# Kernel tuning notes

Measured on AMD Instinct MI355X. Metric: run time of the kernel, lower is better.

The kernel has to match this reference:

```python
import jax, jax.numpy as jnp
import numpy as np

N = 50000        # num_nodes
E = 800000       # num edges (avg degree 16)
R = 8            # num_relations
D_IN = 128       # input_dim
D_H = 128        # gnn_dim
D_OUT = 128      # embed_dim
NUM_DRUGS = 4000 # nodes with node_type == 0 used for pairing
P = 8192         # number of drug pairs (edge_filter columns)


def setup_inputs() -> dict:
    key = jax.random.key(0)
    ks = jax.random.split(key, 24)
    s = 0.05

    def w(k, shape):
        return jax.random.normal(k, shape, jnp.float32) * s

    inp = {
        "x": jax.random.normal(ks[0], (N, D_IN), jnp.float32),
        "edge_index": jax.random.randint(ks[1], (2, E), 0, N),
        "edge_type": jax.random.randint(ks[2], (E,), 0, R),
        "node_type": jax.random.randint(ks[3], (N,), 0, 2),
        "edge_filter": jax.random.randint(ks[4], (2, P), 0, NUM_DRUGS),
        # RGCN layer 1/2/3: per-relation weights, root weight, bias
        "W1": w(ks[5], (R, D_IN, D_H)), "root1": w(ks[6], (D_IN, D_H)), "b1": jnp.zeros((D_H,), jnp.float32),
        "W2": w(ks[7], (R, D_H, D_H)),  "root2": w(ks[8], (D_H, D_H)),  "b2": jnp.zeros((D_H,), jnp.float32),
        "W3": w(ks[9], (R, D_H, D_H)),  "root3": w(ks[10], (D_H, D_H)), "b3": jnp.zeros((D_H,), jnp.float32),
        # ComboMLP: Bilinear(d,d,d) + 3-layer MLP
        "bil_W": w(ks[11], (D_H, D_H, D_H)), "bil_b": jnp.zeros((D_H,), jnp.float32),
        "m1_W": w(ks[12], (D_H, D_H)), "m1_b": jnp.zeros((D_H,), jnp.float32),
        "m2_W": w(ks[13], (D_H, D_H)), "m2_b": jnp.zeros((D_H,), jnp.float32),
        "m3_W": w(ks[14], (D_H, D_OUT)), "m3_b": jnp.zeros((D_OUT,), jnp.float32),
    }
    return inp


def _rgcn_layer(x, src, dst, etype, W, root, b):
    # PyG RGCNConv with aggr='mean': per relation r, mean of neighbor
    # features over incoming rel-r edges, transformed by W[r]; plus root + bias.
    d = x.shape[1]
    msgs = x[src]                                   # [E, d] gather
    seg = dst * R + etype                           # per-(node, relation) segment id
    agg = jax.ops.segment_sum(msgs, seg, num_segments=N * R).reshape(N, R, d)
    cnt = jax.ops.segment_sum(jnp.ones_like(etype, jnp.float32), seg,
                              num_segments=N * R).reshape(N, R, 1)
    mean = agg / jnp.maximum(cnt, 1.0)              # nodes w/o rel-r edges -> 0
    return jnp.einsum('nrd,rde->ne', mean, W) + x @ root + b


def reference(x, edge_index, edge_type, node_type, edge_filter,
              W1, root1, b1, W2, root2, b2, W3, root3, b3,
              bil_W, bil_b, m1_W, m1_b, m2_W, m2_b, m3_W, m3_b):
    src, dst = edge_index[0], edge_index[1]
    h = jax.nn.relu(_rgcn_layer(x, src, dst, edge_type, W1, root1, b1))
    h = jax.nn.relu(_rgcn_layer(h, src, dst, edge_type, W2, root2, b2))
    h = jax.nn.relu(_rgcn_layer(h, src, dst, edge_type, W3, root3, b3))

    # drug_embeds = kg_out[where(node_type == 0)] (fixed-size for jit)
    drug_idx = jnp.nonzero(node_type == 0, size=NUM_DRUGS, fill_value=0)[0]
    drug = h[drug_idx]                              # [NUM_DRUGS, d]
    fa = drug[edge_filter[0]]                       # [P, d]
    fb = drug[edge_filter[1]]                       # [P, d]

    # torch.nn.Bilinear: out[p,o] = fa[p] @ bil_W[o] @ fb[p] + bil_b[o]
    x_ab = jax.nn.relu(jnp.einsum('pi,oij,pj->po', fa, bil_W, fb) + bil_b)
    x_ab = jax.nn.relu(x_ab @ m1_W + m1_b)
    x_ab = jax.nn.relu(x_ab @ m2_W + m2_b)
    return x_ab @ m3_W + m3_b                       # [P, D_OUT]
```

## Files before the change

### kernel.cpp

```cpp
#include <hip/hip_runtime.h>
#include <hip/hip_bf16.h>

typedef unsigned short ushort_t;
typedef __attribute__((ext_vector_type(8))) short short8v;
typedef __attribute__((ext_vector_type(4))) float f32x4;
typedef __attribute__((ext_vector_type(4))) int int4v;

#define NN 50000
#define EE 800000
#define RRR 8
#define DD 128
#define NDRUG 4000
#define PPAIR 8192
#define BML 32
#define AFS 1160

__device__ __forceinline__ float bf2f(ushort_t u) {
    unsigned int v = ((unsigned int)u) << 16;
    float f; __builtin_memcpy(&f, &v, 4); return f;
}
__device__ __forceinline__ ushort_t f2bf(float f) {
    unsigned int b; __builtin_memcpy(&b, &f, 4);
    unsigned int r = (b + 0x7FFFu + ((b >> 16) & 1u)) >> 16;
    return (ushort_t)r;
}
__device__ __forceinline__ unsigned int pkbf(float lo, float hi) {
    unsigned int r;
    asm("v_cvt_pk_bf16_f32 %0, %1, %2" : "=v"(r) : "v"(lo), "v"(hi));
    return r;
}


__global__ __launch_bounds__(256) void k_count(const int* __restrict__ ei,
                                               const int* __restrict__ et,
                                               int* __restrict__ cnt) {
    int e = blockIdx.x * 256 + threadIdx.x;
    if (e < EE) {
        int dst = ei[EE + e];
        atomicAdd(&cnt[dst * RRR + et[e]], 1);
    }
}

__global__ __launch_bounds__(256) void k_inv_indeg(const int* __restrict__ cnt,
                                                   float* __restrict__ inv,
                                                   int* __restrict__ indeg) {
    int n = blockIdx.x * 256 + threadIdx.x;
    if (n < NN) {
        int s = 0;
#pragma unroll
        for (int r = 0; r < RRR; r++) {
            int c = cnt[n * RRR + r];
            s += c;
            inv[n * RRR + r] = 1.0f / (float)(c > 0 ? c : 1);
        }
        indeg[n] = s;
    }
}

__global__ __launch_bounds__(1024) void k_scan_sel(const int* __restrict__ indeg,
                                                   const int* __restrict__ ntype,
                                                   int* __restrict__ offs,
                                                   int* __restrict__ cursor,
                                                   int* __restrict__ didx) {
    __shared__ int w1[16], w2[16];
    __shared__ int sb1, sb2;
    int tid = threadIdx.x, wid = tid >> 6, lane = tid & 63;
    if (tid == 0) { sb1 = 0; sb2 = 0; }
    __syncthreads();
    for (int c0 = 0; c0 < NN; c0 += 1024) {
        int i = c0 + tid;
        int a0 = (i < NN) ? indeg[i] : 0;
        int b0 = (i < NN && ntype[i] == 0) ? 1 : 0;
        int a = a0, b = b0;
#pragma unroll
        for (int off = 1; off < 64; off <<= 1) {
            int ua = __shfl_up(a, off);
            int ub = __shfl_up(b, off);
            if (lane >= off) { a += ua; b += ub; }
        }
        if (lane == 63) { w1[wid] = a; w2[wid] = b; }
        __syncthreads();
        if (wid == 0) {
            int wa = (lane < 16) ? w1[lane] : 0;
            int wb = (lane < 16) ? w2[lane] : 0;
#pragma unroll
            for (int off = 1; off < 16; off <<= 1) {
                int ua = __shfl_up(wa, off);
                int ub = __shfl_up(wb, off);
                if (lane >= off) { wa += ua; wb += ub; }
            }
            if (lane < 16) { w1[lane] = wa; w2[lane] = wb; }
        }
        __syncthreads();
        int ea = sb1 + (wid ? w1[wid - 1] : 0) + (a - a0);
        int eb = sb2 + (wid ? w2[wid - 1] : 0) + (b - b0);
        if (i < NN) { offs[i] = ea; cursor[i] = ea; }
        if (b0 && eb < NDRUG) didx[eb] = i;
        __syncthreads();
        if (tid == 0) { sb1 += w1[15]; sb2 += w2[15]; }
        __syncthreads();
    }
    if (tid == 0) offs[NN] = sb1;
}

__global__ __launch_bounds__(256) void k_scatter(const int* __restrict__ ei,
                                                 const int* __restrict__ et,
                                                 int* __restrict__ cursor,
                                                 int* __restrict__ sorted) {
    int e = blockIdx.x * 256 + threadIdx.x;
    if (e < EE) {
        int dst = ei[EE + e];
        int pos = atomicAdd(&cursor[dst], 1);
        sorted[pos] = ei[e] | (et[e] << 20);
    }
}


__global__ __launch_bounds__(256) void k_cvt(const float* __restrict__ src,
                                             ushort_t* __restrict__ dst, int n4) {
    int i = blockIdx.x * 256 + threadIdx.x;
    if (i < n4) {
        float4 v = ((const float4*)src)[i];
        uint2 o;
        o.x = (unsigned int)f2bf(v.x) | ((unsigned int)f2bf(v.y) << 16);
        o.y = (unsigned int)f2bf(v.z) | ((unsigned int)f2bf(v.w) << 16);
        ((uint2*)dst)[i] = o;
    }
}

__global__ __launch_bounds__(256) void k_prep_wcat(const float* __restrict__ W8,
                                                   const float* __restrict__ root,
                                                   ushort_t* __restrict__ dst) {
    int idx = blockIdx.x * 256 + threadIdx.x;
    if (idx < 144 * 128 * 8) {
        int e = idx & 7, col = (idx >> 3) & 127, ko = idx >> 10;
        int k = ko * 8 + e, slab = k >> 7, kk = k & 127;
        const float* src = (slab < 8) ? (W8 + slab * 16384) : root;
        dst[idx] = f2bf(src[kk * 128 + col]);
    }
}

__global__ __launch_bounds__(256) void k_prep_w(const float* __restrict__ root,
                                                ushort_t* __restrict__ dst) {
    int idx = blockIdx.x * 256 + threadIdx.x;
    if (idx < 16384) {
        int col = idx >> 7, kk = idx & 127;
        dst[idx] = f2bf(root[kk * 128 + col]);
    }
}

__global__ __launch_bounds__(256) void k_prep_wb3(const float* __restrict__ bilW,
                                                  ushort_t* __restrict__ dst) {
    int idx = blockIdx.x * 256 + threadIdx.x;
    if (idx < 2097152) {
        int e = idx & 7, o = (idx >> 3) & 127, ko = idx >> 10;
        dst[idx] = f2bf(bilW[(size_t)o * 16384 + ko * 8 + e]);
    }
}

__global__ __launch_bounds__(512) void k_layer(const ushort_t* __restrict__ hin,
                                               const ushort_t* __restrict__ WcatT,
                                               const float* __restrict__ bias,
                                               const float* __restrict__ inv,
                                               const int* __restrict__ offs,
                                               const int* __restrict__ sorted,
                                               ushort_t* __restrict__ hout) {
    __shared__ short Af[BML * AFS];
    int tid = threadIdx.x;
    int n0 = blockIdx.x * BML;
    int node = tid >> 4, tsub = tid & 15;
    int n = n0 + node;

    float acc[8][8];
#pragma unroll
    for (int r = 0; r < 8; r++)
#pragma unroll
        for (int q = 0; q < 8; q++) acc[r][q] = 0.f;
    short8v hv = {0, 0, 0, 0, 0, 0, 0, 0};

    if (n < NN) {
        hv = ((const short8v*)hin)[(size_t)n * 16 + tsub];
        int e0 = offs[n], e1 = offs[n + 1];
        for (int e = e0; e < e1; e++) {
            int pk = sorted[e];
            int src = pk & 0xFFFFF;
            int et = pk >> 20;
            union { int4v v; short s[8]; } u;
            u.v = ((const int4v*)hin)[(size_t)src * 16 + tsub];
            float v[8];
#pragma unroll
            for (int q = 0; q < 8; q++) v[q] = bf2f((ushort_t)u.s[q]);
#define CASE_R(R) case R: _Pragma("unroll") for (int q = 0; q < 8; q++) acc[R][q] += v[q]; break;
            switch (et) {
                CASE_R(0) CASE_R(1) CASE_R(2) CASE_R(3)
                CASE_R(4) CASE_R(5) CASE_R(6) CASE_R(7)
            }
#undef CASE_R
        }
    }
    int nc = (n < NN) ? n : (NN - 1);
#pragma unroll
    for (int slab = 0; slab < 8; slab++) {
        float sc = (n < NN) ? inv[nc * 8 + slab] : 0.f;
        union { unsigned int u[4]; short8v v; } cv;
        cv.u[0] = pkbf(acc[slab][0] * sc, acc[slab][1] * sc);
        cv.u[1] = pkbf(acc[slab][2] * sc, acc[slab][3] * sc);
        cv.u[2] = pkbf(acc[slab][4] * sc, acc[slab][5] * sc);
        cv.u[3] = pkbf(acc[slab][6] * sc, acc[slab][7] * sc);
        *(short8v*)&Af[node * AFS + slab * 128 + tsub * 8] = cv.v;
    }
    *(short8v*)&Af[node * AFS + 1024 + tsub * 8] = hv;
    __syncthreads();

    int wid = tid >> 6, lane = tid & 63, lo = lane & 15, hi = lane >> 4;
    int rhalf = wid & 1, cgrp = wid >> 1;
    int arow = rhalf * 16 + lo;
    f32x4 a0v = {0.f, 0.f, 0.f, 0.f}, a1v = {0.f, 0.f, 0.f, 0.f};
    const int4v* Bg = (const int4v*)WcatT;
#pragma unroll
    for (int kc = 0; kc < 9; kc++) {
#pragma unroll
        for (int s = 0; s < 4; s++) {
            short8v a = *(const short8v*)&Af[arow * AFS + kc * 128 + s * 32 + hi * 8];
            int ko = kc * 16 + s * 4 + hi;
            union { int4v i; short8v s8; } b0, b1;
            b0.i = Bg[ko * 128 + cgrp * 32 + lo];
            b1.i = Bg[ko * 128 + cgrp * 32 + 16 + lo];
            a0v = __builtin_amdgcn_mfma_f32_16x16x32_bf16(a, b0.s8, a0v, 0, 0, 0);
            a1v = __builtin_amdgcn_mfma_f32_16x16x32_bf16(a, b1.s8, a1v, 0, 0, 0);
        }
    }
#pragma unroll
    for (int q = 0; q < 4; q++) {
        int r = n0 + rhalf * 16 + hi * 4 + q;
        if (r < NN) {
            int c = cgrp * 32 + lo;
            float v0 = fmaxf(a0v[q] + bias[c], 0.f);
            float v1 = fmaxf(a1v[q] + bias[c + 16], 0.f);
            hout[(size_t)r * 128 + c] = f2bf(v0);
            hout[(size_t)r * 128 + c + 16] = f2bf(v1);
        }
    }
}

__global__ __launch_bounds__(256) void k_mfma_nn(const ushort_t* __restrict__ A,
                                                 const ushort_t* __restrict__ Wt,
                                                 const float* __restrict__ bias,
                                                 ushort_t* __restrict__ outb,
                                                 float* __restrict__ outf,
                                                 int M, int nMblk, int relu) {
    __shared__ short As[64 * 136];
    __shared__ short Bs[128 * 136];
    int tid = threadIdx.x;
    int mblk = blockIdx.x % nMblk;
    int row0 = mblk * 64;

    const int4v* Ag = (const int4v*)A;
    int4v* AsV = (int4v*)As;
    for (int idx = tid; idx < 1024; idx += 256) {
        int row = idx >> 4, ck = idx & 15;
        int grow = row0 + row;
        int4v v = {0, 0, 0, 0};
        if (grow < M) v = Ag[(size_t)grow * 16 + ck];
        AsV[row * 17 + ck] = v;
    }
    const int4v* Wg = (const int4v*)Wt;
    int4v* BsV = (int4v*)Bs;
    for (int idx = tid; idx < 2048; idx += 256) {
        int col = idx >> 4, ck = idx & 15;
        BsV[col * 17 + ck] = Wg[idx];
    }
    __syncthreads();

    int wid = tid >> 6, lane = tid & 63, lo = lane & 15, hi = lane >> 4;
    int wrow0 = wid * 16;
    f32x4 acc[8];
#pragma unroll
    for (int t = 0; t < 8; t++) acc[t] = (f32x4)(0.f);

#pragma unroll
    for (int s = 0; s < 4; ++s) {
        short8v a = *(const short8v*)&As[(wrow0 + lo) * 136 + s * 32 + hi * 8];
#pragma unroll
        for (int t = 0; t < 8; t++) {
            short8v b = *(const short8v*)&Bs[(t * 16 + lo) * 136 + s * 32 + hi * 8];
            acc[t] = __builtin_amdgcn_mfma_f32_16x16x32_bf16(a, b, acc[t], 0, 0, 0);
        }
    }

#pragma unroll
    for (int t = 0; t < 8; t++) {
        int col = t * 16 + lo;
        float bs = bias ? bias[col] : 0.f;
#pragma unroll
        for (int q = 0; q < 4; q++) {
            int grow = row0 + wrow0 + hi * 4 + q;
            if (grow < M) {
                float v = acc[t][q] + bs;
                if (relu) v = fmaxf(v, 0.f);
                size_t oidx = (size_t)grow * 128 + col;
                if (outb) outb[oidx] = f2bf(v);
                else      outf[oidx] = v;
            }
        }
    }
}

__global__ __launch_bounds__(512) void k_bil(const ushort_t* __restrict__ hb,
                                             const int* __restrict__ didx,
                                             const int* __restrict__ efil,
                                             const ushort_t* __restrict__ Wb,
                                             const float* __restrict__ bilb,
                                             ushort_t* __restrict__ xab) {
    __shared__ __align__(16) char smem[65536];
    __shared__ int pa[32], pb[32];
    float* faT = (float*)smem;
    float* fbF = (float*)(smem + 16896);
    int tid = threadIdx.x;
    int p0 = blockIdx.x * 32;

    if (tid < 32) pa[tid] = didx[efil[p0 + tid]];
    else if (tid < 64) pb[tid - 32] = didx[efil[PPAIR + p0 + tid - 32]];
    __syncthreads();

    {
        int p = tid >> 4, c8 = tid & 15;
        const int4v* hg = (const int4v*)hb;
        union { int4v v; short s[8]; } ra, rb;
        ra.v = hg[(size_t)pa[p] * 16 + c8];
        rb.v = hg[(size_t)pb[p] * 16 + c8];
        float4* fb4 = (float4*)fbF;
        float4 f0, f1;
        f0.x = bf2f((ushort_t)rb.s[0]); f0.y = bf2f((ushort_t)rb.s[1]);
        f0.z = bf2f((ushort_t)rb.s[2]); f0.w = bf2f((ushort_t)rb.s[3]);
        f1.x = bf2f((ushort_t)rb.s[4]); f1.y = bf2f((ushort_t)rb.s[5]);
        f1.z = bf2f((ushort_t)rb.s[6]); f1.w = bf2f((ushort_t)rb.s[7]);
        fb4[p * 33 + c8 * 2] = f0;
        fb4[p * 33 + c8 * 2 + 1] = f1;
#pragma unroll
        for (int j = 0; j < 8; j++)
            faT[(c8 * 8 + j) * 33 + p] = bf2f((ushort_t)ra.s[j]);
    }
    __syncthreads();

    int wid = tid >> 6, lane = tid & 63, lo = lane & 15, hi = lane >> 4;
    const int4v* Wbg = (const int4v*)Wb;
    const float4* fb4 = (const float4*)fbF;

    f32x4 acc0[8], acc1[8];
#pragma unroll
    for (int t = 0; t < 8; t++) { acc0[t] = (f32x4)(0.f); acc1[t] = (f32x4)(0.f); }

    for (int s = 0; s < 64; ++s) {
        int ko = (wid << 8) + (s << 2) + hi;
        int4v braw[8];
#pragma unroll
        for (int t = 0; t < 8; t++)
            braw[t] = Wbg[ko * 128 + t * 16 + lo];

        int i = (wid << 4) + (s >> 2);
        int jc4 = ((s & 3) << 3) + (hi << 1);
        short8v afr0, afr1;
#pragma unroll
        for (int mi = 0; mi < 2; ++mi) {
            int prow = (mi << 4) + lo;
            float fa = faT[i * 33 + prow];
            float4 f0 = fb4[prow * 33 + jc4];
            float4 f1 = fb4[prow * 33 + jc4 + 1];
            union { unsigned int u[4]; short8v v; } cv;
            cv.u[0] = pkbf(fa * f0.x, fa * f0.y);
            cv.u[1] = pkbf(fa * f0.z, fa * f0.w);
            cv.u[2] = pkbf(fa * f1.x, fa * f1.y);
            cv.u[3] = pkbf(fa * f1.z, fa * f1.w);
            if (mi == 0) afr0 = cv.v; else afr1 = cv.v;
        }
#pragma unroll
        for (int t = 0; t < 8; t++) {
            union { int4v i4; short8v s8; } bb; bb.i4 = braw[t];
            acc0[t] = __builtin_amdgcn_mfma_f32_16x16x32_bf16(afr0, bb.s8, acc0[t], 0, 0, 0);
            acc1[t] = __builtin_amdgcn_mfma_f32_16x16x32_bf16(afr1, bb.s8, acc1[t], 0, 0, 0);
        }
    }
    __syncthreads();

    float* redF = (float*)smem;
    if (wid >= 4) {
        float* r = redF + (wid - 4) * 4096;
#pragma unroll
        for (int t = 0; t < 8; t++)
#pragma unroll
            for (int q = 0; q < 4; q++) {
                r[(hi * 4 + q) * 128 + t * 16 + lo] = acc0[t][q];
                r[(16 + hi * 4 + q) * 128 + t * 16 + lo] = acc1[t][q];
            }
    }
    __syncthreads();
    if (wid < 4) {
        float* r = redF + wid * 4096;
#pragma unroll
        for (int t = 0; t < 8; t++)
#pragma unroll
            for (int q = 0; q < 4; q++) {
                acc0[t][q] += r[(hi * 4 + q) * 128 + t * 16 + lo];
                acc1[t][q] += r[(16 + hi * 4 + q) * 128 + t * 16 + lo];
            }
    }
    __syncthreads();
    if (wid < 4) {
        float* r = redF + wid * 4096;
#pragma unroll
        for (int t = 0; t < 8; t++)
#pragma unroll
            for (int q = 0; q < 4; q++) {
                r[(hi * 4 + q) * 128 + t * 16 + lo] = acc0[t][q];
                r[(16 + hi * 4 + q) * 128 + t * 16 + lo] = acc1[t][q];
            }
    }
    __syncthreads();
    for (int idx = tid; idx < 4096; idx += 512) {
        float s = redF[idx] + redF[4096 + idx] + redF[8192 + idx] + redF[12288 + idx]
                + bilb[idx & 127];
        s = fmaxf(s, 0.f);
        xab[(size_t)(p0 + (idx >> 7)) * 128 + (idx & 127)] = f2bf(s);
    }
}


extern "C" void kernel_launch(void* const* d_in, const int* in_sizes, int n_in,
                              void* d_out, int out_size, void* d_ws, size_t ws_size,
                              hipStream_t stream) {
    const float* x      = (const float*)d_in[0];
    const int*   ei     = (const int*)d_in[1];
    const int*   et     = (const int*)d_in[2];
    const int*   ntype  = (const int*)d_in[3];
    const int*   efil   = (const int*)d_in[4];
    const float* W1 = (const float*)d_in[5];
    const float* r1 = (const float*)d_in[6];
    const float* b1 = (const float*)d_in[7];
    const float* W2 = (const float*)d_in[8];
    const float* r2 = (const float*)d_in[9];
    const float* b2 = (const float*)d_in[10];
    const float* W3 = (const float*)d_in[11];
    const float* r3 = (const float*)d_in[12];
    const float* b3 = (const float*)d_in[13];
    const float* bilW = (const float*)d_in[14];
    const float* bilb = (const float*)d_in[15];
    const float* m1W = (const float*)d_in[16];
    const float* m1b = (const float*)d_in[17];
    const float* m2W = (const float*)d_in[18];
    const float* m2b = (const float*)d_in[19];
    const float* m3W = (const float*)d_in[20];
    const float* m3b = (const float*)d_in[21];
    float* outp = (float*)d_out;

    char* ws = (char*)d_ws;
    size_t off = 0;
    auto alloc = [&](size_t bytes) { size_t c = off; off = (off + bytes + 255) & ~(size_t)255; return c; };

    size_t oxb   = alloc((size_t)NN * 128 * 2);
    size_t ohA   = alloc((size_t)NN * 128 * 2);
    size_t ohB   = alloc((size_t)NN * 128 * 2);
    size_t oWc1  = alloc((size_t)144 * 128 * 8 * 2);
    size_t oWc2  = alloc((size_t)144 * 128 * 8 * 2);
    size_t oWc3  = alloc((size_t)144 * 128 * 8 * 2);
    size_t omW1  = alloc((size_t)16384 * 2);
    size_t omW2  = alloc((size_t)16384 * 2);
    size_t omW3  = alloc((size_t)16384 * 2);
    size_t oWb   = alloc((size_t)2097152 * 2);
    size_t oxab1 = alloc((size_t)PPAIR * 128 * 2);
    size_t oxab2 = alloc((size_t)PPAIR * 128 * 2);
    size_t ocnt  = alloc((size_t)NN * RRR * sizeof(int));
    size_t oinv  = alloc((size_t)NN * RRR * sizeof(float));
    size_t oindeg = alloc((size_t)NN * sizeof(int));
    size_t ooffs = alloc((size_t)(NN + 1) * sizeof(int));
    size_t ocur  = alloc((size_t)NN * sizeof(int));
    size_t osort = alloc((size_t)EE * sizeof(int));
    size_t odidx = alloc((size_t)NDRUG * sizeof(int));

    ushort_t* xb   = (ushort_t*)(ws + oxb);
    ushort_t* hbA  = (ushort_t*)(ws + ohA);
    ushort_t* hbB  = (ushort_t*)(ws + ohB);
    ushort_t* Wc1  = (ushort_t*)(ws + oWc1);
    ushort_t* Wc2  = (ushort_t*)(ws + oWc2);
    ushort_t* Wc3  = (ushort_t*)(ws + oWc3);
    ushort_t* mWt1 = (ushort_t*)(ws + omW1);
    ushort_t* mWt2 = (ushort_t*)(ws + omW2);
    ushort_t* mWt3 = (ushort_t*)(ws + omW3);
    ushort_t* Wb3  = (ushort_t*)(ws + oWb);
    ushort_t* xab1 = (ushort_t*)(ws + oxab1);
    ushort_t* xab2 = (ushort_t*)(ws + oxab2);
    int*      cnt  = (int*)(ws + ocnt);
    float*    inv  = (float*)(ws + oinv);
    int*      indeg = (int*)(ws + oindeg);
    int*      offs = (int*)(ws + ooffs);
    int*      cursor = (int*)(ws + ocur);
    int*      sorted = (int*)(ws + osort);
    int*      didx = (int*)(ws + odidx);

    hipMemsetAsync(cnt, 0, (size_t)NN * RRR * sizeof(int), stream);
    hipMemsetAsync(didx, 0, (size_t)NDRUG * sizeof(int), stream);

    k_cvt<<<(NN * 128 / 4 + 255) / 256, 256, 0, stream>>>(x, xb, NN * 128 / 4);
    k_prep_wcat<<<(144 * 128 * 8 + 255) / 256, 256, 0, stream>>>(W1, r1, Wc1);
    k_prep_wcat<<<(144 * 128 * 8 + 255) / 256, 256, 0, stream>>>(W2, r2, Wc2);
    k_prep_wcat<<<(144 * 128 * 8 + 255) / 256, 256, 0, stream>>>(W3, r3, Wc3);
    k_prep_w<<<(16384 + 255) / 256, 256, 0, stream>>>(m1W, mWt1);
    k_prep_w<<<(16384 + 255) / 256, 256, 0, stream>>>(m2W, mWt2);
    k_prep_w<<<(16384 + 255) / 256, 256, 0, stream>>>(m3W, mWt3);
    k_prep_wb3<<<(2097152 + 255) / 256, 256, 0, stream>>>(bilW, Wb3);

    k_count<<<(EE + 255) / 256, 256, 0, stream>>>(ei, et, cnt);
    k_inv_indeg<<<(NN + 255) / 256, 256, 0, stream>>>(cnt, inv, indeg);
    k_scan_sel<<<1, 1024, 0, stream>>>(indeg, ntype, offs, cursor, didx);
    k_scatter<<<(EE + 255) / 256, 256, 0, stream>>>(ei, et, cursor, sorted);

    const int NBL = (NN + BML - 1) / BML;

    k_layer<<<NBL, 512, 0, stream>>>(xb,  Wc1, b1, inv, offs, sorted, hbA);
    k_layer<<<NBL, 512, 0, stream>>>(hbA, Wc2, b2, inv, offs, sorted, hbB);
    k_layer<<<NBL, 512, 0, stream>>>(hbB, Wc3, b3, inv, offs, sorted, hbA);

    k_bil<<<PPAIR / 32, 512, 0, stream>>>(hbA, didx, efil, Wb3, bilb, xab1);
    const int nMblkP = PPAIR / 64;
    k_mfma_nn<<<nMblkP, 256, 0, stream>>>(xab1, mWt1, m1b, xab2, nullptr, PPAIR, nMblkP, 1);
    k_mfma_nn<<<nMblkP, 256, 0, stream>>>(xab2, mWt2, m2b, xab1, nullptr, PPAIR, nMblkP, 1);
    k_mfma_nn<<<nMblkP, 256, 0, stream>>>(xab1, mWt3, m3b, nullptr, outp, PPAIR, nMblkP, 0);
}
```

Baseline: 728.9 us.

## Bucket CSR edges by source-node window to improve gather locality

Edges are now sorted first by source window (src>>13, 7 windows) and then by destination, giving a windowed CSR with a multi-block parallel scan over 7*N counters. Each layer's aggregation loop walks the windows in order, so concurrently running blocks tend to gather from the same ~8K-node slice of the feature table and get better L2 reuse. The single-block serial scan is replaced by a three-kernel parallel scan plus a separate drug-select kernel. In exchange it adds a second atomic counter array, more offset reads per node, and extra launches.

```diff
diff --git a/kernel.cpp b/kernel.cpp
--- a/kernel.cpp
+++ b/kernel.cpp
@@ -14,6 +14,8 @@
 #define PPAIR 8192
 #define BML 32
 #define AFS 1160
+#define NW 7
+#define SCAN_N (NW * NN)
 
 __device__ __forceinline__ float bf2f(ushort_t u) {
     unsigned int v = ((unsigned int)u) << 16;
@@ -33,74 +35,131 @@
 
 __global__ __launch_bounds__(256) void k_count(const int* __restrict__ ei,
                                                const int* __restrict__ et,
-                                               int* __restrict__ cnt) {
+                                               int* __restrict__ cnt,
+                                               int* __restrict__ cnt2) {
     int e = blockIdx.x * 256 + threadIdx.x;
     if (e < EE) {
+        int src = ei[e];
         int dst = ei[EE + e];
         atomicAdd(&cnt[dst * RRR + et[e]], 1);
-    }
-}
-
-__global__ __launch_bounds__(256) void k_inv_indeg(const int* __restrict__ cnt,
-                                                   float* __restrict__ inv,
-                                                   int* __restrict__ indeg) {
+        atomicAdd(&cnt2[(src >> 13) * NN + dst], 1);
+    }
+}
+
+__global__ __launch_bounds__(256) void k_inv(const int* __restrict__ cnt,
+                                             float* __restrict__ inv) {
     int n = blockIdx.x * 256 + threadIdx.x;
     if (n < NN) {
-        int s = 0;
 #pragma unroll
         for (int r = 0; r < RRR; r++) {
             int c = cnt[n * RRR + r];
-            s += c;
             inv[n * RRR + r] = 1.0f / (float)(c > 0 ? c : 1);
         }
-        indeg[n] = s;
-    }
-}
-
-__global__ __launch_bounds__(1024) void k_scan_sel(const int* __restrict__ indeg,
-                                                   const int* __restrict__ ntype,
-                                                   int* __restrict__ offs,
-                                                   int* __restrict__ cursor,
-                                                   int* __restrict__ didx) {
-    __shared__ int w1[16], w2[16];
-    __shared__ int sb1, sb2;
+    }
+}
+
+__global__ __launch_bounds__(1024) void k_scanA(const int* __restrict__ cnt2,
+                                                int* __restrict__ offs,
+                                                int* __restrict__ part) {
+    __shared__ int ws[16];
     int tid = threadIdx.x, wid = tid >> 6, lane = tid & 63;
-    if (tid == 0) { sb1 = 0; sb2 = 0; }
+    int i = blockIdx.x * 1024 + tid;
+    int v0 = (i < SCAN_N) ? cnt2[i] : 0;
+    int v = v0;
+#pragma unroll
+    for (int off = 1; off < 64; off <<= 1) {
+        int u = __shfl_up(v, off);
+        if (lane >= off) v += u;
+    }
+    if (lane == 63) ws[wid] = v;
+    __syncthreads();
+    if (wid == 0) {
+        int wv = (lane < 16) ? ws[lane] : 0;
+#pragma unroll
+        for (int off = 1; off < 16; off <<= 1) {
+            int u = __shfl_up(wv, off);
+            if (lane >= off) wv += u;
+        }
+        if (lane < 16) ws[lane] = wv;
+    }
+    __syncthreads();
+    int excl = (wid ? ws[wid - 1] : 0) + (v - v0);
+    if (i < SCAN_N) offs[i] = excl;
+    if (tid == 0) part[blockIdx.x] = ws[15];
+}
+
+__global__ __launch_bounds__(512) void k_scanB(int* __restrict__ part, int nPart) {
+    __shared__ int ws[8];
+    int tid = threadIdx.x, wid = tid >> 6, lane = tid & 63;
+    int p0 = (tid < nPart) ? part[tid] : 0;
+    int p = p0;
+#pragma unroll
+    for (int off = 1; off < 64; off <<= 1) {
+        int u = __shfl_up(p, off);
+        if (lane >= off) p += u;
+    }
+    if (lane == 63) ws[wid] = p;
+    __syncthreads();
+    if (wid == 0) {
+        int wv = (lane < 8) ? ws[lane] : 0;
+#pragma unroll
+        for (int off = 1; off < 8; off <<= 1) {
+            int u = __shfl_up(wv, off);
+            if (lane >= off) wv += u;
+        }
+        if (lane < 8) ws[lane] = wv;
+    }
+    __syncthreads();
+    int excl = (wid ? ws[wid - 1] : 0) + (p - p0);
+    if (tid < nPart) part[tid] = excl;
+}
+
+__global__ __launch_bounds__(1024) void k_scanC(int* __restrict__ offs,
+                                                const int* __restrict__ part,
+                                                int* __restrict__ cursor) {
+    int i = blockIdx.x * 1024 + threadIdx.x;
+    if (i < SCAN_N) {
+        int v = offs[i] + part[blockIdx.x];
+        offs[i] = v;
+        cursor[i] = v;
+    }
+    if (i == SCAN_N) offs[SCAN_N] = EE;
+}
+
+__global__ __launch_bounds__(1024) void k_select(const int* __restrict__ ntype,
+                                                 int* __restrict__ didx) {
+    __shared__ int ws[16];
+    __shared__ int sbase;
+    int tid = threadIdx.x, wid = tid >> 6, lane = tid & 63;
+    if (tid == 0) sbase = 0;
     __syncthreads();
     for (int c0 = 0; c0 < NN; c0 += 1024) {
         int i = c0 + tid;
-        int a0 = (i < NN) ? indeg[i] : 0;
-        int b0 = (i < NN && ntype[i] == 0) ? 1 : 0;
-        int a = a0, b = b0;
+        int v0 = (i < NN && ntype[i] == 0) ? 1 : 0;
+        int v = v0;
 #pragma unroll
         for (int off = 1; off < 64; off <<= 1) {
-            int ua = __shfl_up(a, off);
-            int ub = __shfl_up(b, off);
-            if (lane >= off) { a += ua; b += ub; }
-        }
-        if (lane == 63) { w1[wid] = a; w2[wid] = b; }
+            int u = __shfl_up(v, off);
+            if (lane >= off) v += u;
+        }
+        if (lane == 63) ws[wid] = v;
         __syncthreads();
         if (wid == 0) {
-            int wa = (lane < 16) ? w1[lane] : 0;
-            int wb = (lane < 16) ? w2[lane] : 0;
+            int wv = (lane < 16) ? ws[lane] : 0;
 #pragma unroll
             for (int off = 1; off < 16; off <<= 1) {
-                int ua = __shfl_up(wa, off);
-                int ub = __shfl_up(wb, off);
-                if (lane >= off) { wa += ua; wb += ub; }
+                int u = __shfl_up(wv, off);
+                if (lane >= off) wv += u;
             }
-            if (lane < 16) { w1[lane] = wa; w2[lane] = wb; }
+            if (lane < 16) ws[lane] = wv;
         }
         __syncthreads();
-        int ea = sb1 + (wid ? w1[wid - 1] : 0) + (a - a0);
-        int eb = sb2 + (wid ? w2[wid - 1] : 0) + (b - b0);
-        if (i < NN) { offs[i] = ea; cursor[i] = ea; }
-        if (b0 && eb < NDRUG) didx[eb] = i;
+        int excl = sbase + (wid ? ws[wid - 1] : 0) + (v - v0);
+        if (v0 && excl < NDRUG) didx[excl] = i;
         __syncthreads();
-        if (tid == 0) { sb1 += w1[15]; sb2 += w2[15]; }
+        if (tid == 0) sbase += ws[15];
         __syncthreads();
     }
-    if (tid == 0) offs[NN] = sb1;
 }
 
 __global__ __launch_bounds__(256) void k_scatter(const int* __restrict__ ei,
@@ -109,9 +168,10 @@
                                                  int* __restrict__ sorted) {
     int e = blockIdx.x * 256 + threadIdx.x;
     if (e < EE) {
+        int src = ei[e];
         int dst = ei[EE + e];
-        int pos = atomicAdd(&cursor[dst], 1);
-        sorted[pos] = ei[e] | (et[e] << 20);
+        int pos = atomicAdd(&cursor[(src >> 13) * NN + dst], 1);
+        sorted[pos] = src | (et[e] << 20);
     }
 }
 
@@ -162,7 +222,7 @@
                                                const ushort_t* __restrict__ WcatT,
                                                const float* __restrict__ bias,
                                                const float* __restrict__ inv,
-                                               const int* __restrict__ offs,
+                                               const int* __restrict__ offsW,
                                                const int* __restrict__ sorted,
                                                ushort_t* __restrict__ hout) {
     __shared__ short Af[BML * AFS];
@@ -180,22 +240,26 @@
 
     if (n < NN) {
         hv = ((const short8v*)hin)[(size_t)n * 16 + tsub];
-        int e0 = offs[n], e1 = offs[n + 1];
-        for (int e = e0; e < e1; e++) {
-            int pk = sorted[e];
-            int src = pk & 0xFFFFF;
-            int et = pk >> 20;
-            union { int4v v; short s[8]; } u;
-            u.v = ((const int4v*)hin)[(size_t)src * 16 + tsub];
-            float v[8];
-#pragma unroll
-            for (int q = 0; q < 8; q++) v[q] = bf2f((ushort_t)u.s[q]);
+        const int4v* hg = (const int4v*)hin;
+        for (int w = 0; w < NW; w++) {
+            int e0 = offsW[w * NN + n];
+            int e1 = offsW[w * NN + n + 1];
+            for (int e = e0; e < e1; e++) {
+                int pk = sorted[e];
+                int src = pk & 0xFFFFF;
+                int et = pk >> 20;
+                union { int4v v; short s[8]; } u;
+                u.v = hg[(size_t)src * 16 + tsub];
+                float v[8];
+#pragma unroll
+                for (int q = 0; q < 8; q++) v[q] = bf2f((ushort_t)u.s[q]);
 #define CASE_R(R) case R: _Pragma("unroll") for (int q = 0; q < 8; q++) acc[R][q] += v[q]; break;
-            switch (et) {
-                CASE_R(0) CASE_R(1) CASE_R(2) CASE_R(3)
-                CASE_R(4) CASE_R(5) CASE_R(6) CASE_R(7)
+                switch (et) {
+                    CASE_R(0) CASE_R(1) CASE_R(2) CASE_R(3)
+                    CASE_R(4) CASE_R(5) CASE_R(6) CASE_R(7)
+                }
+#undef CASE_R
             }
-#undef CASE_R
         }
     }
     int nc = (n < NN) ? n : (NN - 1);
@@ -457,6 +521,8 @@
     size_t off = 0;
     auto alloc = [&](size_t bytes) { size_t c = off; off = (off + bytes + 255) & ~(size_t)255; return c; };
 
+    const int nScanBlk = (SCAN_N + 1023) / 1024;
+
     size_t oxb   = alloc((size_t)NN * 128 * 2);
     size_t ohA   = alloc((size_t)NN * 128 * 2);
     size_t ohB   = alloc((size_t)NN * 128 * 2);
@@ -470,10 +536,11 @@
     size_t oxab1 = alloc((size_t)PPAIR * 128 * 2);
     size_t oxab2 = alloc((size_t)PPAIR * 128 * 2);
     size_t ocnt  = alloc((size_t)NN * RRR * sizeof(int));
+    size_t ocnt2 = alloc((size_t)SCAN_N * sizeof(int));
     size_t oinv  = alloc((size_t)NN * RRR * sizeof(float));
-    size_t oindeg = alloc((size_t)NN * sizeof(int));
-    size_t ooffs = alloc((size_t)(NN + 1) * sizeof(int));
-    size_t ocur  = alloc((size_t)NN * sizeof(int));
+    size_t ooffs = alloc((size_t)(SCAN_N + 1) * sizeof(int));
+    size_t ocur  = alloc((size_t)SCAN_N * sizeof(int));
+    size_t opart = alloc((size_t)512 * sizeof(int));
     size_t osort = alloc((size_t)EE * sizeof(int));
     size_t odidx = alloc((size_t)NDRUG * sizeof(int));
 
@@ -490,14 +557,16 @@
     ushort_t* xab1 = (ushort_t*)(ws + oxab1);
     ushort_t* xab2 = (ushort_t*)(ws + oxab2);
     int*      cnt  = (int*)(ws + ocnt);
+    int*      cnt2 = (int*)(ws + ocnt2);
     float*    inv  = (float*)(ws + oinv);
-    int*      indeg = (int*)(ws + oindeg);
-    int*      offs = (int*)(ws + ooffs);
+    int*      offsW = (int*)(ws + ooffs);
     int*      cursor = (int*)(ws + ocur);
+    int*      part = (int*)(ws + opart);
     int*      sorted = (int*)(ws + osort);
     int*      didx = (int*)(ws + odidx);
 
     hipMemsetAsync(cnt, 0, (size_t)NN * RRR * sizeof(int), stream);
+    hipMemsetAsync(cnt2, 0, (size_t)SCAN_N * sizeof(int), stream);
     hipMemsetAsync(didx, 0, (size_t)NDRUG * sizeof(int), stream);
 
     k_cvt<<<(NN * 128 / 4 + 255) / 256, 256, 0, stream>>>(x, xb, NN * 128 / 4);
@@ -509,16 +578,19 @@
     k_prep_w<<<(16384 + 255) / 256, 256, 0, stream>>>(m3W, mWt3);
     k_prep_wb3<<<(2097152 + 255) / 256, 256, 0, stream>>>(bilW, Wb3);
 
-    k_count<<<(EE + 255) / 256, 256, 0, stream>>>(ei, et, cnt);
-    k_inv_indeg<<<(NN + 255) / 256, 256, 0, stream>>>(cnt, inv, indeg);
-    k_scan_sel<<<1, 1024, 0, stream>>>(indeg, ntype, offs, cursor, didx);
+    k_count<<<(EE + 255) / 256, 256, 0, stream>>>(ei, et, cnt, cnt2);
+    k_inv<<<(NN + 255) / 256, 256, 0, stream>>>(cnt, inv);
+    k_scanA<<<nScanBlk, 1024, 0, stream>>>(cnt2, offsW, part);
+    k_scanB<<<1, 512, 0, stream>>>(part, nScanBlk);
+    k_scanC<<<nScanBlk + 1, 1024, 0, stream>>>(offsW, part, cursor);
+    k_select<<<1, 1024, 0, stream>>>(ntype, didx);
     k_scatter<<<(EE + 255) / 256, 256, 0, stream>>>(ei, et, cursor, sorted);
 
     const int NBL = (NN + BML - 1) / BML;
 
-    k_layer<<<NBL, 512, 0, stream>>>(xb,  Wc1, b1, inv, offs, sorted, hbA);
-    k_layer<<<NBL, 512, 0, stream>>>(hbA, Wc2, b2, inv, offs, sorted, hbB);
-    k_layer<<<NBL, 512, 0, stream>>>(hbB, Wc3, b3, inv, offs, sorted, hbA);
+    k_layer<<<NBL, 512, 0, stream>>>(xb,  Wc1, b1, inv, offsW, sorted, hbA);
+    k_layer<<<NBL, 512, 0, stream>>>(hbA, Wc2, b2, inv, offsW, sorted, hbB);
+    k_layer<<<NBL, 512, 0, stream>>>(hbB, Wc3, b3, inv, offsW, sorted, hbA);
 
     k_bil<<<PPAIR / 32, 512, 0, stream>>>(hbA, didx, efil, Wb3, bilb, xab1);
     const int nMblkP = PPAIR / 64;
```

Measured after the change: 803.3 us. 1.1x slower.
